# Kernel tuning notes

Hardware: AMD Instinct MI355X
Metric: run time of the kernel (lower is better)

The kernel has to match this reference:

```python
import jax, jax.numpy as jnp
import numpy as np

N, T, P, H, K = 10000, 64, 64, 128, 32
K1, K2 = K // 2, K - K // 2
C = P // 2  # GAT out_channels
E = 320000
EPS = 1e-5


def gru_layer(x, Wih, Whh, bih, bhh):
    # x: [N, T, in]; PyTorch GRU cell semantics
    Hd = Whh.shape[1]
    def step(h, xt):
        gi = xt @ Wih.T + bih            # [N, 3H]
        gh = h @ Whh.T + bhh
        i_r, i_z, i_n = jnp.split(gi, 3, axis=-1)
        h_r, h_z, h_n = jnp.split(gh, 3, axis=-1)
        r = jax.nn.sigmoid(i_r + h_r)
        z = jax.nn.sigmoid(i_z + h_z)
        n = jnp.tanh(i_n + r * h_n)
        h_new = (1.0 - z) * n + z * h
        return h_new, h_new
    h0 = jnp.zeros((x.shape[0], Hd), x.dtype)
    _, ys = jax.lax.scan(step, h0, jnp.swapaxes(x, 0, 1))
    return jnp.swapaxes(ys, 0, 1)


def gru2_last(x, p0, p1):
    y0 = gru_layer(x, *p0)
    y1 = gru_layer(y0, *p1)
    return y1[:, -1, :]


def gat_conv(x, edge_index, W, att_src, att_dst, bias):
    # PyG GATConv, heads=1, concat=False, add_self_loops=True, slope=0.2
    n = x.shape[0]
    h = x @ W                                   # [N, C]
    loops = jnp.arange(n)
    src = jnp.concatenate([edge_index[0], loops])
    dst = jnp.concatenate([edge_index[1], loops])
    a_s = h @ att_src                            # [N]
    a_d = h @ att_dst
    e = jax.nn.leaky_relu(a_s[src] + a_d[dst], 0.2)
    emax = jax.lax.stop_gradient(jax.ops.segment_max(e, dst, num_segments=n))
    ex = jnp.exp(e - emax[dst])
    denom = jax.ops.segment_sum(ex, dst, num_segments=n)
    alpha = ex / denom[dst]
    out = jax.ops.segment_sum(alpha[:, None] * h[src], dst, num_segments=n)
    return out + bias


def batchnorm(x, g, b):
    m = jnp.mean(x, axis=0)
    v = jnp.var(x, axis=0)
    return (x - m) * jax.lax.rsqrt(v + EPS) * g + b


def setup_inputs() -> dict:
    key = jax.random.key(0)
    ks = jax.random.split(key, 40)
    s = 0.05
    d = {}
    d["X_seq"] = jax.random.normal(ks[0], (N, T, P), jnp.float32)
    d["edge_index"] = jax.random.randint(ks[1], (2, E), 0, N, jnp.int64)
    i = 2
    for name, ind in (("gru_t", P), ("gru_cs", P)):
        for l, fin in ((0, ind), (1, H)):
            d[f"{name}_Wih{l}"] = jax.random.normal(ks[i], (3 * H, fin)) * s; i += 1
            d[f"{name}_Whh{l}"] = jax.random.normal(ks[i], (3 * H, H)) * s; i += 1
            d[f"{name}_bih{l}"] = jax.random.normal(ks[i], (3 * H,)) * s; i += 1
            d[f"{name}_bhh{l}"] = jax.random.normal(ks[i], (3 * H,)) * s; i += 1
    d["gat_W"] = jax.random.normal(ks[i], (P, C)) * s; i += 1
    d["gat_att_src"] = jax.random.normal(ks[i], (C,)) * s; i += 1
    d["gat_att_dst"] = jax.random.normal(ks[i], (C,)) * s; i += 1
    d["gat_bias"] = jax.random.normal(ks[i], (C,)) * s; i += 1
    d["proj_t_W"] = jax.random.normal(ks[i], (K1, H)) * s; i += 1
    d["proj_t_b"] = jax.random.normal(ks[i], (K1,)) * s; i += 1
    d["proj_cs_W"] = jax.random.normal(ks[i], (K2, H)) * s; i += 1
    d["proj_cs_b"] = jax.random.normal(ks[i], (K2,)) * s; i += 1
    d["bn1_g"] = jnp.ones((K1,)); d["bn1_b"] = jnp.zeros((K1,))
    d["bn2_g"] = jnp.ones((K2,)); d["bn2_b"] = jnp.zeros((K2,))
    return d


def reference(X_seq, edge_index,
              gru_t_Wih0, gru_t_Whh0, gru_t_bih0, gru_t_bhh0,
              gru_t_Wih1, gru_t_Whh1, gru_t_bih1, gru_t_bhh1,
              gru_cs_Wih0, gru_cs_Whh0, gru_cs_bih0, gru_cs_bhh0,
              gru_cs_Wih1, gru_cs_Whh1, gru_cs_bih1, gru_cs_bhh1,
              gat_W, gat_att_src, gat_att_dst, gat_bias,
              proj_t_W, proj_t_b, proj_cs_W, proj_cs_b,
              bn1_g, bn1_b, bn2_g, bn2_b):
    h_t = gru2_last(X_seq,
                    (gru_t_Wih0, gru_t_Whh0, gru_t_bih0, gru_t_bhh0),
                    (gru_t_Wih1, gru_t_Whh1, gru_t_bih1, gru_t_bhh1))
    X_t = X_seq[:, -1, :]                            # [N, P]
    gat_out = gat_conv(X_t, edge_index, gat_W, gat_att_src, gat_att_dst, gat_bias)
    pad = jnp.zeros((X_t.shape[0], P - C), X_t.dtype)
    residual = X_t - jnp.concatenate([gat_out, pad], axis=1)
    h_cs = gru2_last(residual[:, None, :],
                     (gru_cs_Wih0, gru_cs_Whh0, gru_cs_bih0, gru_cs_bhh0),
                     (gru_cs_Wih1, gru_cs_Whh1, gru_cs_bih1, gru_cs_bhh1))
    f1 = batchnorm(h_t @ proj_t_W.T + proj_t_b, bn1_g, bn1_b)
    f2 = batchnorm(h_cs @ proj_cs_W.T + proj_cs_b, bn2_g, bn2_b)
    return jnp.concatenate([f1, f2], axis=1)
```

## Files before the change

### kernel.cpp

```cpp
#include <hip/hip_runtime.h>
#include <hip/hip_fp16.h>

#define NN 10000
#define TT 64
#define PP 64
#define HH 128
#define EE 320000

typedef _Float16 half8 __attribute__((ext_vector_type(8)));
typedef float f32x4 __attribute__((ext_vector_type(4)));

__device__ __forceinline__ float sigm(float x) {
    return __builtin_amdgcn_rcpf(1.0f + __expf(-x));
}
__device__ __forceinline__ float tanh_(float x) {
    return 1.0f - 2.0f * __builtin_amdgcn_rcpf(__expf(2.0f * x) + 1.0f);
}
__device__ __forceinline__ int hswz(int row, int colbyte) {
    return row * 256 + (colbyte ^ ((row & 7) << 4));
}

__global__ void pack_w_kernel(const float* __restrict__ Wa, int Ka,
                              const float* __restrict__ Wb,
                              _Float16* __restrict__ out, int total) {
    int idx = blockIdx.x * 256 + threadIdx.x;
    if (idx >= total) return;
    int K = Ka + HH;
    int r = idx / K, k = idx - r * K;
    float v = (k < Ka) ? Wa[r * Ka + k] : Wb[r * HH + (k - Ka)];
    out[idx] = (_Float16)v;
}

__global__ __launch_bounds__(512, 2) void gru2_t8_kernel(
    const float* __restrict__ x, int T, int xstride,
    const _Float16* __restrict__ W0,
    const float* __restrict__ bih0, const float* __restrict__ bhh0,
    const _Float16* __restrict__ W1,
    const float* __restrict__ bih1, const float* __restrict__ bhh1,
    float* __restrict__ hout)
{
    __shared__ __align__(16) char lds[65536];
    char* const WX = lds + 16384;
    const int tid = threadIdx.x;
    const int wv = tid >> 6;
    const int lane = tid & 63;
    const int l15 = lane & 15, lg = lane >> 4;
    const int rowbase = blockIdx.x * 16;
    const int col = wv * 16 + l15;

    for (int i = tid; i < 4096; i += 512) ((int*)lds)[i] = 0;

    #pragma unroll
    for (int g = 0; g < 3; ++g) {
        const _Float16* r0 = W0 + ((size_t)((g * 8 + wv) * 16 + l15)) * 192;
        #pragma unroll
        for (int kt = 0; kt < 2; ++kt)
            *(half8*)(WX + wv * 6144 + (g * 2 + kt) * 1024 + lane * 16) =
                *(const half8*)(r0 + kt * 32 + lg * 8);
    }

    half8 w0h[3][4], w1[3][8];
    #pragma unroll
    for (int g = 0; g < 3; ++g) {
        const _Float16* r0 = W0 + ((size_t)((g * 8 + wv) * 16 + l15)) * 192;
        #pragma unroll
        for (int kt = 0; kt < 4; ++kt) w0h[g][kt] = *(const half8*)(r0 + 64 + kt * 32 + lg * 8);
        const _Float16* r1 = W1 + ((size_t)((g * 8 + wv) * 16 + l15)) * 256;
        #pragma unroll
        for (int kt = 0; kt < 8; ++kt) w1[g][kt] = *(const half8*)(r1 + kt * 32 + lg * 8);
    }
    #pragma unroll
    for (int g = 0; g < 3; ++g) {
        #pragma unroll
        for (int kt = 0; kt < 4; ++kt) asm volatile("" : "+a"(w0h[g][kt]));
        #pragma unroll
        for (int kt = 0; kt < 8; ++kt) asm volatile("" : "+a"(w1[g][kt]));
    }

    const float br0  = bih0[col] + bhh0[col];
    const float bz0  = bih0[128 + col] + bhh0[128 + col];
    const float bni0 = bih0[256 + col];
    const float bnh0 = bhh0[256 + col];
    const float br1  = bih1[col] + bhh1[col];
    const float bz1  = bih1[128 + col] + bhh1[128 + col];
    const float bni1 = bih1[256 + col];
    const float bnh1 = bhh1[256 + col];

    const float* xr = x + (size_t)(rowbase + l15) * xstride;

    float hp0[4] = {0.f, 0.f, 0.f, 0.f};
    float hp1[4] = {0.f, 0.f, 0.f, 0.f};

    __syncthreads();

    for (int it = 0; it <= T; ++it) {
        const int off = (it & 1) * 4096;
        char* const H0r = lds + off;
        char* const H0w = lds + (4096 - off);
        char* const H1r = lds + 8192 + off;
        char* const H1w = lds + 8192 + (4096 - off);

        float4 xu0, xv0, xu1, xv1;
        if (it < T) {
            const float* p = xr + it * PP;
            xu0 = *(const float4*)(p + lg * 8);
            xv0 = *(const float4*)(p + lg * 8 + 4);
            xu1 = *(const float4*)(p + 32 + lg * 8);
            xv1 = *(const float4*)(p + 32 + lg * 8 + 4);
        }

        if (it >= 1) {
            f32x4 ar  = {br1, br1, br1, br1};
            f32x4 az  = {bz1, bz1, bz1, bz1};
            f32x4 ani = {bni1, bni1, bni1, bni1};
            f32x4 anh = {bnh1, bnh1, bnh1, bnh1};
            #pragma unroll
            for (int kt = 0; kt < 4; ++kt) {
                const int boff = (kt * 32 + lg * 8) * 2;
                half8 ay  = *(const half8*)(H0r + hswz(l15, boff));
                half8 ah1 = *(const half8*)(H1r + hswz(l15, boff));
                ar  = __builtin_amdgcn_mfma_f32_16x16x32_f16(ay,  w1[0][kt],   ar, 0,0,0);
                ar  = __builtin_amdgcn_mfma_f32_16x16x32_f16(ah1, w1[0][4+kt], ar, 0,0,0);
                az  = __builtin_amdgcn_mfma_f32_16x16x32_f16(ay,  w1[1][kt],   az, 0,0,0);
                az  = __builtin_amdgcn_mfma_f32_16x16x32_f16(ah1, w1[1][4+kt], az, 0,0,0);
                ani = __builtin_amdgcn_mfma_f32_16x16x32_f16(ay,  w1[2][kt],   ani, 0,0,0);
                anh = __builtin_amdgcn_mfma_f32_16x16x32_f16(ah1, w1[2][4+kt], anh, 0,0,0);
            }
            #pragma unroll
            for (int r = 0; r < 4; ++r) {
                float rg = sigm(ar[r]);
                float zg = sigm(az[r]);
                float ng = tanh_(ani[r] + rg * anh[r]);
                float hv = ng + zg * (hp1[r] - ng);
                hp1[r] = hv;
                *(_Float16*)(H1w + hswz(lg * 4 + r, col * 2)) = (_Float16)hv;
            }
        }

        if (it < T) {
            half8 ax0, ax1;
            ax0[0]=(_Float16)xu0.x; ax0[1]=(_Float16)xu0.y; ax0[2]=(_Float16)xu0.z; ax0[3]=(_Float16)xu0.w;
            ax0[4]=(_Float16)xv0.x; ax0[5]=(_Float16)xv0.y; ax0[6]=(_Float16)xv0.z; ax0[7]=(_Float16)xv0.w;
            ax1[0]=(_Float16)xu1.x; ax1[1]=(_Float16)xu1.y; ax1[2]=(_Float16)xu1.z; ax1[3]=(_Float16)xu1.w;
            ax1[4]=(_Float16)xv1.x; ax1[5]=(_Float16)xv1.y; ax1[6]=(_Float16)xv1.z; ax1[7]=(_Float16)xv1.w;
            f32x4 ar  = {br0, br0, br0, br0};
            f32x4 az  = {bz0, bz0, bz0, bz0};
            f32x4 ani = {bni0, bni0, bni0, bni0};
            f32x4 anh = {bnh0, bnh0, bnh0, bnh0};
            #pragma unroll
            for (int kt = 0; kt < 2; ++kt) {
                const char* wb = WX + wv * 6144 + kt * 1024 + lane * 16;
                half8 wxr = *(const half8*)(wb);
                half8 wxz = *(const half8*)(wb + 2048);
                half8 wxn = *(const half8*)(wb + 4096);
                half8 ax = (kt == 0) ? ax0 : ax1;
                ar  = __builtin_amdgcn_mfma_f32_16x16x32_f16(ax, wxr, ar, 0,0,0);
                az  = __builtin_amdgcn_mfma_f32_16x16x32_f16(ax, wxz, az, 0,0,0);
                ani = __builtin_amdgcn_mfma_f32_16x16x32_f16(ax, wxn, ani, 0,0,0);
            }
            #pragma unroll
            for (int kt = 0; kt < 4; ++kt) {
                half8 ah = *(const half8*)(H0r + hswz(l15, (kt * 32 + lg * 8) * 2));
                ar  = __builtin_amdgcn_mfma_f32_16x16x32_f16(ah, w0h[0][kt], ar, 0,0,0);
                az  = __builtin_amdgcn_mfma_f32_16x16x32_f16(ah, w0h[1][kt], az, 0,0,0);
                anh = __builtin_amdgcn_mfma_f32_16x16x32_f16(ah, w0h[2][kt], anh, 0,0,0);
            }
            #pragma unroll
            for (int r = 0; r < 4; ++r) {
                float rg = sigm(ar[r]);
                float zg = sigm(az[r]);
                float ng = tanh_(ani[r] + rg * anh[r]);
                float hv = ng + zg * (hp0[r] - ng);
                hp0[r] = hv;
                *(_Float16*)(H0w + hswz(lg * 4 + r, col * 2)) = (_Float16)hv;
            }
        }
        __syncthreads();
    }

    #pragma unroll
    for (int r = 0; r < 4; ++r)
        hout[(size_t)(rowbase + lg * 4 + r) * HH + col] = hp1[r];
}

__global__ void gat_node_kernel(const float* __restrict__ Xseq, const float* __restrict__ W,
                                const float* __restrict__ att_s, const float* __restrict__ att_d,
                                float* __restrict__ h, float* __restrict__ a_s, float* __restrict__ a_d,
                                float* __restrict__ denom, float* __restrict__ accum) {
    __shared__ float sW[64][33];
    __shared__ float sas[32], sad[32];
    int tid = threadIdx.x;
    for (int i = tid; i < 64 * 32; i += 256) sW[i >> 5][i & 31] = W[i];
    if (tid < 32) { sas[tid] = att_s[tid]; sad[tid] = att_d[tid]; }
    __syncthreads();
    int c = tid & 31;
    int n = blockIdx.x * 8 + (tid >> 5);
    const float* xr = Xseq + (size_t)n * (TT * PP) + 63 * PP;
    float acc = 0.f;
    #pragma unroll
    for (int k = 0; k < 64; ++k) acc += xr[k] * sW[k][c];
    h[n * 32 + c] = acc;
    accum[n * 32 + c] = 0.f;
    float ps = acc * sas[c];
    float pd = acc * sad[c];
    #pragma unroll
    for (int m = 16; m > 0; m >>= 1) { ps += __shfl_xor(ps, m, 32); pd += __shfl_xor(pd, m, 32); }
    if (c == 0) { a_s[n] = ps; a_d[n] = pd; denom[n] = 0.f; }
}

__global__ void gat_edge_kernel(const int* __restrict__ ei,
                                const float* __restrict__ a_s, const float* __restrict__ a_d,
                                const float* __restrict__ h,
                                float* __restrict__ denom, float* __restrict__ accum) {
    int gid = blockIdx.x * 256 + threadIdx.x;
    int e = gid >> 5, c = gid & 31;
    if (e >= EE + NN) return;
    int src, dst;
    if (e < EE) { src = ei[e]; dst = ei[EE + e]; }
    else        { src = e - EE; dst = src; }
    float s = a_s[src] + a_d[dst];
    float le = (s > 0.f) ? s : 0.2f * s;
    float ex = __expf(le);
    unsafeAtomicAdd(&accum[dst * 32 + c], ex * h[src * 32 + c]);
    if (c == 0) unsafeAtomicAdd(&denom[dst], ex);
}

__global__ void residual_kernel(const float* __restrict__ Xseq, const float* __restrict__ accum,
                                const float* __restrict__ denom, const float* __restrict__ bias,
                                float* __restrict__ res) {
    int idx = blockIdx.x * 256 + threadIdx.x;
    if (idx >= NN * 64) return;
    int n = idx >> 6, k = idx & 63;
    float xv = Xseq[(size_t)n * (TT * PP) + 63 * PP + k];
    float g = 0.f;
    if (k < 32) g = accum[n * 32 + k] / denom[n] + bias[k];
    res[idx] = xv - g;
}

__global__ void proj_kernel(const float* __restrict__ ht, const float* __restrict__ hcs,
                            const float* __restrict__ Wt, const float* __restrict__ bt,
                            const float* __restrict__ Wc, const float* __restrict__ bc,
                            float* __restrict__ out) {
    __shared__ float sW[32][129];
    __shared__ float sb[32];
    int tid = threadIdx.x;
    for (int i = tid; i < 16 * 128; i += 256) {
        sW[i >> 7][i & 127] = Wt[i];
        sW[16 + (i >> 7)][i & 127] = Wc[i];
    }
    if (tid < 16) { sb[tid] = bt[tid]; sb[16 + tid] = bc[tid]; }
    __syncthreads();
    int idx = blockIdx.x * 256 + tid;
    int n = idx >> 5, c = idx & 31;
    const float* hrow = ((c < 16) ? ht : hcs) + (size_t)n * HH;
    const float* wrow = sW[c];
    float acc = sb[c];
    #pragma unroll 8
    for (int k = 0; k < 128; ++k) acc += hrow[k] * wrow[k];
    out[idx] = acc;
}

__global__ void bn_stats_kernel(const float* __restrict__ raw,
                                const float* __restrict__ g1, const float* __restrict__ b1,
                                const float* __restrict__ g2, const float* __restrict__ b2,
                                float* __restrict__ ss) {
    int c = blockIdx.x;
    int tid = threadIdx.x;
    float s = 0.f, q = 0.f;
    for (int n = tid; n < NN; n += 256) {
        float v = raw[n * 32 + c];
        s += v; q += v * v;
    }
    __shared__ float ls[256], lq[256];
    ls[tid] = s; lq[tid] = q;
    __syncthreads();
    for (int st = 128; st > 0; st >>= 1) {
        if (tid < st) { ls[tid] += ls[tid + st]; lq[tid] += lq[tid + st]; }
        __syncthreads();
    }
    if (tid == 0) {
        float m = ls[0] / (float)NN;
        float var = lq[0] / (float)NN - m * m;
        float istd = rsqrtf(var + 1e-5f);
        float gg = (c < 16) ? g1[c] : g2[c - 16];
        float bb = (c < 16) ? b1[c] : b2[c - 16];
        float sc = istd * gg;
        ss[c] = sc;
        ss[32 + c] = bb - m * sc;
    }
}

__global__ void bn_apply_kernel(float* __restrict__ out, const float* __restrict__ ss) {
    int idx = blockIdx.x * 256 + threadIdx.x;
    if (idx >= NN * 32) return;
    int c = idx & 31;
    out[idx] = out[idx] * ss[c] + ss[32 + c];
}

extern "C" void kernel_launch(void* const* d_in, const int* in_sizes, int n_in,
                              void* d_out, int out_size, void* d_ws, size_t ws_size,
                              hipStream_t stream) {
    const float* Xseq  = (const float*)d_in[0];
    const int*   ei    = (const int*)d_in[1];
    const float* tWih0 = (const float*)d_in[2];
    const float* tWhh0 = (const float*)d_in[3];
    const float* tbih0 = (const float*)d_in[4];
    const float* tbhh0 = (const float*)d_in[5];
    const float* tWih1 = (const float*)d_in[6];
    const float* tWhh1 = (const float*)d_in[7];
    const float* tbih1 = (const float*)d_in[8];
    const float* tbhh1 = (const float*)d_in[9];
    const float* cWih0 = (const float*)d_in[10];
    const float* cWhh0 = (const float*)d_in[11];
    const float* cbih0 = (const float*)d_in[12];
    const float* cbhh0 = (const float*)d_in[13];
    const float* cWih1 = (const float*)d_in[14];
    const float* cWhh1 = (const float*)d_in[15];
    const float* cbih1 = (const float*)d_in[16];
    const float* cbhh1 = (const float*)d_in[17];
    const float* gatW  = (const float*)d_in[18];
    const float* atts  = (const float*)d_in[19];
    const float* attd  = (const float*)d_in[20];
    const float* gatb  = (const float*)d_in[21];
    const float* ptW   = (const float*)d_in[22];
    const float* ptb   = (const float*)d_in[23];
    const float* pcW   = (const float*)d_in[24];
    const float* pcb   = (const float*)d_in[25];
    const float* bn1g  = (const float*)d_in[26];
    const float* bn1b  = (const float*)d_in[27];
    const float* bn2g  = (const float*)d_in[28];
    const float* bn2b  = (const float*)d_in[29];

    char* ws = (char*)d_ws;
    _Float16* Wt0 = (_Float16*)(ws);
    _Float16* Wt1 = (_Float16*)(ws + 147456);
    _Float16* Wc0 = (_Float16*)(ws + 344064);
    _Float16* Wc1 = (_Float16*)(ws + 491520);
    float* h_t   = (float*)(ws + 688128);
    float* h_cs  = (float*)(ws + 5808128);
    float* gath  = (float*)(ws + 10928128);
    float* a_s   = (float*)(ws + 12208128);
    float* a_d   = (float*)(ws + 12248128);
    float* denom = (float*)(ws + 12288128);
    float* accum = (float*)(ws + 12328128);
    float* resid = (float*)(ws + 13608128);
    float* ss    = (float*)(ws + 16168128);

    pack_w_kernel<<<288, 256, 0, stream>>>(tWih0, 64,  tWhh0, Wt0, 384 * 192);
    pack_w_kernel<<<384, 256, 0, stream>>>(tWih1, 128, tWhh1, Wt1, 384 * 256);
    pack_w_kernel<<<288, 256, 0, stream>>>(cWih0, 64,  cWhh0, Wc0, 384 * 192);
    pack_w_kernel<<<384, 256, 0, stream>>>(cWih1, 128, cWhh1, Wc1, 384 * 256);

    gru2_t8_kernel<<<625, 512, 0, stream>>>(Xseq, TT, TT * PP, Wt0, tbih0, tbhh0,
                                            Wt1, tbih1, tbhh1, h_t);

    gat_node_kernel<<<1250, 256, 0, stream>>>(Xseq, gatW, atts, attd, gath, a_s, a_d, denom, accum);
    gat_edge_kernel<<<41250, 256, 0, stream>>>(ei, a_s, a_d, gath, denom, accum);
    residual_kernel<<<2500, 256, 0, stream>>>(Xseq, accum, denom, gatb, resid);

    gru2_t8_kernel<<<625, 512, 0, stream>>>(resid, 1, PP, Wc0, cbih0, cbhh0,
                                            Wc1, cbih1, cbhh1, h_cs);

    proj_kernel<<<1250, 256, 0, stream>>>(h_t, h_cs, ptW, ptb, pcW, pcb, (float*)d_out);
    bn_stats_kernel<<<32, 256, 0, stream>>>((const float*)d_out, bn1g, bn1b, bn2g, bn2b, ss);
    bn_apply_kernel<<<1250, 256, 0, stream>>>((float*)d_out, ss);
}
```

Before: 528.4 us.

## Process 48 rows per GRU block to amortize register-resident weights

Each GRU block now handles three 16-row M-fragments (48 rows) instead of one, reusing the register- and LDS-resident weights across more rows per sync step. The launch drops from 625 to 209 blocks and uses 96KB of dynamic LDS, with launch bounds lowered to one block per SIMD set. The previous hidden state is now read back from LDS in fp16 instead of kept in fp32 registers, which frees registers but adds rounding of the recurrent state. With 209 blocks on a 256-CU part, some CUs sit idle and occupancy is lower, so latency hiding depends on the three independent fragments.

After: 765.0 us. 1.45x slower.

```diff
diff --git a/kernel.cpp b/kernel.cpp
--- a/kernel.cpp
+++ b/kernel.cpp
@@ -31,7 +31,7 @@
     out[idx] = (_Float16)v;
 }
 
-__global__ __launch_bounds__(512, 2) void gru2_t8_kernel(
+__global__ __launch_bounds__(512, 1) void gru2_t8_kernel(
     const float* __restrict__ x, int T, int xstride,
     const _Float16* __restrict__ W0,
     const float* __restrict__ bih0, const float* __restrict__ bhh0,
@@ -39,16 +39,18 @@
     const float* __restrict__ bih1, const float* __restrict__ bhh1,
     float* __restrict__ hout)
 {
-    __shared__ __align__(16) char lds[65536];
-    char* const WX = lds + 16384;
+    extern __shared__ __align__(16) char lds[];
+    char* const H0B = lds;
+    char* const H1B = lds + 24576;
+    char* const WX  = lds + 49152;
     const int tid = threadIdx.x;
     const int wv = tid >> 6;
     const int lane = tid & 63;
     const int l15 = lane & 15, lg = lane >> 4;
-    const int rowbase = blockIdx.x * 16;
+    const int rowbase = blockIdx.x * 48;
     const int col = wv * 16 + l15;
 
-    for (int i = tid; i < 4096; i += 512) ((int*)lds)[i] = 0;
+    for (int i = tid; i < 12288; i += 512) ((int*)lds)[i] = 0;
 
     #pragma unroll
     for (int g = 0; g < 3; ++g) {
@@ -86,101 +88,111 @@
     const float bni1 = bih1[256 + col];
     const float bnh1 = bhh1[256 + col];
 
-    const float* xr = x + (size_t)(rowbase + l15) * xstride;
-
-    float hp0[4] = {0.f, 0.f, 0.f, 0.f};
-    float hp1[4] = {0.f, 0.f, 0.f, 0.f};
+    const float* xr[3];
+    #pragma unroll
+    for (int mf = 0; mf < 3; ++mf) {
+        int rr = rowbase + mf * 16 + l15;
+        if (rr > NN - 1) rr = NN - 1;
+        xr[mf] = x + (size_t)rr * xstride;
+    }
 
     __syncthreads();
 
     for (int it = 0; it <= T; ++it) {
-        const int off = (it & 1) * 4096;
-        char* const H0r = lds + off;
-        char* const H0w = lds + (4096 - off);
-        char* const H1r = lds + 8192 + off;
-        char* const H1w = lds + 8192 + (4096 - off);
-
-        float4 xu0, xv0, xu1, xv1;
-        if (it < T) {
-            const float* p = xr + it * PP;
-            xu0 = *(const float4*)(p + lg * 8);
-            xv0 = *(const float4*)(p + lg * 8 + 4);
-            xu1 = *(const float4*)(p + 32 + lg * 8);
-            xv1 = *(const float4*)(p + 32 + lg * 8 + 4);
-        }
-
-        if (it >= 1) {
-            f32x4 ar  = {br1, br1, br1, br1};
-            f32x4 az  = {bz1, bz1, bz1, bz1};
-            f32x4 ani = {bni1, bni1, bni1, bni1};
-            f32x4 anh = {bnh1, bnh1, bnh1, bnh1};
-            #pragma unroll
-            for (int kt = 0; kt < 4; ++kt) {
-                const int boff = (kt * 32 + lg * 8) * 2;
-                half8 ay  = *(const half8*)(H0r + hswz(l15, boff));
-                half8 ah1 = *(const half8*)(H1r + hswz(l15, boff));
-                ar  = __builtin_amdgcn_mfma_f32_16x16x32_f16(ay,  w1[0][kt],   ar, 0,0,0);
-                ar  = __builtin_amdgcn_mfma_f32_16x16x32_f16(ah1, w1[0][4+kt], ar, 0,0,0);
-                az  = __builtin_amdgcn_mfma_f32_16x16x32_f16(ay,  w1[1][kt],   az, 0,0,0);
-                az  = __builtin_amdgcn_mfma_f32_16x16x32_f16(ah1, w1[1][4+kt], az, 0,0,0);
-                ani = __builtin_amdgcn_mfma_f32_16x16x32_f16(ay,  w1[2][kt],   ani, 0,0,0);
-                anh = __builtin_amdgcn_mfma_f32_16x16x32_f16(ah1, w1[2][4+kt], anh, 0,0,0);
+        const int off = (it & 1) * 12288;
+        char* const H0r = H0B + off;
+        char* const H0w = H0B + (12288 - off);
+        char* const H1r = H1B + off;
+        char* const H1w = H1B + (12288 - off);
+
+        #pragma unroll
+        for (int mf = 0; mf < 3; ++mf) {
+            const int arow = mf * 16 + l15;
+
+            float4 xu0, xv0, xu1, xv1;
+            if (it < T) {
+                const float* p = xr[mf] + it * PP;
+                xu0 = *(const float4*)(p + lg * 8);
+                xv0 = *(const float4*)(p + lg * 8 + 4);
+                xu1 = *(const float4*)(p + 32 + lg * 8);
+                xv1 = *(const float4*)(p + 32 + lg * 8 + 4);
             }
-            #pragma unroll
-            for (int r = 0; r < 4; ++r) {
-                float rg = sigm(ar[r]);
-                float zg = sigm(az[r]);
-                float ng = tanh_(ani[r] + rg * anh[r]);
-                float hv = ng + zg * (hp1[r] - ng);
-                hp1[r] = hv;
-                *(_Float16*)(H1w + hswz(lg * 4 + r, col * 2)) = (_Float16)hv;
+
+            if (it >= 1) {
+                f32x4 ar  = {br1, br1, br1, br1};
+                f32x4 az  = {bz1, bz1, bz1, bz1};
+                f32x4 ani = {bni1, bni1, bni1, bni1};
+                f32x4 anh = {bnh1, bnh1, bnh1, bnh1};
+                #pragma unroll
+                for (int kt = 0; kt < 4; ++kt) {
+                    const int boff = (kt * 32 + lg * 8) * 2;
+                    half8 ay  = *(const half8*)(H0r + hswz(arow, boff));
+                    half8 ah1 = *(const half8*)(H1r + hswz(arow, boff));
+                    ar  = __builtin_amdgcn_mfma_f32_16x16x32_f16(ay,  w1[0][kt],   ar, 0,0,0);
+                    ar  = __builtin_amdgcn_mfma_f32_16x16x32_f16(ah1, w1[0][4+kt], ar, 0,0,0);
+                    az  = __builtin_amdgcn_mfma_f32_16x16x32_f16(ay,  w1[1][kt],   az, 0,0,0);
+                    az  = __builtin_amdgcn_mfma_f32_16x16x32_f16(ah1, w1[1][4+kt], az, 0,0,0);
+                    ani = __builtin_amdgcn_mfma_f32_16x16x32_f16(ay,  w1[2][kt],   ani, 0,0,0);
+                    anh = __builtin_amdgcn_mfma_f32_16x16x32_f16(ah1, w1[2][4+kt], anh, 0,0,0);
+                }
+                #pragma unroll
+                for (int r = 0; r < 4; ++r) {
+                    const int drow = mf * 16 + lg * 4 + r;
+                    float hold = (float)(*(const _Float16*)(H1r + hswz(drow, col * 2)));
+                    float rg = sigm(ar[r]);
+                    float zg = sigm(az[r]);
+                    float ng = tanh_(ani[r] + rg * anh[r]);
+                    float hv = ng + zg * (hold - ng);
+                    *(_Float16*)(H1w + hswz(drow, col * 2)) = (_Float16)hv;
+                    if (it == T) {
+                        const int grow = rowbase + drow;
+                        if (grow < NN) hout[(size_t)grow * HH + col] = hv;
+                    }
+                }
             }
-        }
-
-        if (it < T) {
-            half8 ax0, ax1;
-            ax0[0]=(_Float16)xu0.x; ax0[1]=(_Float16)xu0.y; ax0[2]=(_Float16)xu0.z; ax0[3]=(_Float16)xu0.w;
-            ax0[4]=(_Float16)xv0.x; ax0[5]=(_Float16)xv0.y; ax0[6]=(_Float16)xv0.z; ax0[7]=(_Float16)xv0.w;
-            ax1[0]=(_Float16)xu1.x; ax1[1]=(_Float16)xu1.y; ax1[2]=(_Float16)xu1.z; ax1[3]=(_Float16)xu1.w;
-            ax1[4]=(_Float16)xv1.x; ax1[5]=(_Float16)xv1.y; ax1[6]=(_Float16)xv1.z; ax1[7]=(_Float16)xv1.w;
-            f32x4 ar  = {br0, br0, br0, br0};
-            f32x4 az  = {bz0, bz0, bz0, bz0};
-            f32x4 ani = {bni0, bni0, bni0, bni0};
-            f32x4 anh = {bnh0, bnh0, bnh0, bnh0};
-            #pragma unroll
-            for (int kt = 0; kt < 2; ++kt) {
-                const char* wb = WX + wv * 6144 + kt * 1024 + lane * 16;
-                half8 wxr = *(const half8*)(wb);
-                half8 wxz = *(const half8*)(wb + 2048);
-                half8 wxn = *(const half8*)(wb + 4096);
-                half8 ax = (kt == 0) ? ax0 : ax1;
-                ar  = __builtin_amdgcn_mfma_f32_16x16x32_f16(ax, wxr, ar, 0,0,0);
-                az  = __builtin_amdgcn_mfma_f32_16x16x32_f16(ax, wxz, az, 0,0,0);
-                ani = __builtin_amdgcn_mfma_f32_16x16x32_f16(ax, wxn, ani, 0,0,0);
-            }
-            #pragma unroll
-            for (int kt = 0; kt < 4; ++kt) {
-                half8 ah = *(const half8*)(H0r + hswz(l15, (kt * 32 + lg * 8) * 2));
-                ar  = __builtin_amdgcn_mfma_f32_16x16x32_f16(ah, w0h[0][kt], ar, 0,0,0);
-                az  = __builtin_amdgcn_mfma_f32_16x16x32_f16(ah, w0h[1][kt], az, 0,0,0);
-                anh = __builtin_amdgcn_mfma_f32_16x16x32_f16(ah, w0h[2][kt], anh, 0,0,0);
-            }
-            #pragma unroll
-            for (int r = 0; r < 4; ++r) {
-                float rg = sigm(ar[r]);
-                float zg = sigm(az[r]);
-                float ng = tanh_(ani[r] + rg * anh[r]);
-                float hv = ng + zg * (hp0[r] - ng);
-                hp0[r] = hv;
-                *(_Float16*)(H0w + hswz(lg * 4 + r, col * 2)) = (_Float16)hv;
+
+            if (it < T) {
+                half8 ax0, ax1;
+                ax0[0]=(_Float16)xu0.x; ax0[1]=(_Float16)xu0.y; ax0[2]=(_Float16)xu0.z; ax0[3]=(_Float16)xu0.w;
+                ax0[4]=(_Float16)xv0.x; ax0[5]=(_Float16)xv0.y; ax0[6]=(_Float16)xv0.z; ax0[7]=(_Float16)xv0.w;
+                ax1[0]=(_Float16)xu1.x; ax1[1]=(_Float16)xu1.y; ax1[2]=(_Float16)xu1.z; ax1[3]=(_Float16)xu1.w;
+                ax1[4]=(_Float16)xv1.x; ax1[5]=(_Float16)xv1.y; ax1[6]=(_Float16)xv1.z; ax1[7]=(_Float16)xv1.w;
+                f32x4 ar  = {br0, br0, br0, br0};
+                f32x4 az  = {bz0, bz0, bz0, bz0};
+                f32x4 ani = {bni0, bni0, bni0, bni0};
+                f32x4 anh = {bnh0, bnh0, bnh0, bnh0};
+                #pragma unroll
+                for (int kt = 0; kt < 2; ++kt) {
+                    const char* wb = WX + wv * 6144 + kt * 1024 + lane * 16;
+                    half8 wxr = *(const half8*)(wb);
+                    half8 wxz = *(const half8*)(wb + 2048);
+                    half8 wxn = *(const half8*)(wb + 4096);
+                    half8 ax = (kt == 0) ? ax0 : ax1;
+                    ar  = __builtin_amdgcn_mfma_f32_16x16x32_f16(ax, wxr, ar, 0,0,0);
+                    az  = __builtin_amdgcn_mfma_f32_16x16x32_f16(ax, wxz, az, 0,0,0);
+                    ani = __builtin_amdgcn_mfma_f32_16x16x32_f16(ax, wxn, ani, 0,0,0);
+                }
+                #pragma unroll
+                for (int kt = 0; kt < 4; ++kt) {
+                    half8 ah = *(const half8*)(H0r + hswz(arow, (kt * 32 + lg * 8) * 2));
+                    ar  = __builtin_amdgcn_mfma_f32_16x16x32_f16(ah, w0h[0][kt], ar, 0,0,0);
+                    az  = __builtin_amdgcn_mfma_f32_16x16x32_f16(ah, w0h[1][kt], az, 0,0,0);
+                    anh = __builtin_amdgcn_mfma_f32_16x16x32_f16(ah, w0h[2][kt], anh, 0,0,0);
+                }
+                #pragma unroll
+                for (int r = 0; r < 4; ++r) {
+                    const int drow = mf * 16 + lg * 4 + r;
+                    float hold = (float)(*(const _Float16*)(H0r + hswz(drow, col * 2)));
+                    float rg = sigm(ar[r]);
+                    float zg = sigm(az[r]);
+                    float ng = tanh_(ani[r] + rg * anh[r]);
+                    float hv = ng + zg * (hold - ng);
+                    *(_Float16*)(H0w + hswz(drow, col * 2)) = (_Float16)hv;
+                }
             }
         }
         __syncthreads();
     }
-
-    #pragma unroll
-    for (int r = 0; r < 4; ++r)
-        hout[(size_t)(rowbase + lg * 4 + r) * HH + col] = hp1[r];
 }
 
 __global__ void gat_node_kernel(const float* __restrict__ Xseq, const float* __restrict__ W,
@@ -346,20 +358,23 @@
     float* resid = (float*)(ws + 13608128);
     float* ss    = (float*)(ws + 16168128);
 
+    (void)hipFuncSetAttribute((const void*)gru2_t8_kernel,
+                              hipFuncAttributeMaxDynamicSharedMemorySize, 98304);
+
     pack_w_kernel<<<288, 256, 0, stream>>>(tWih0, 64,  tWhh0, Wt0, 384 * 192);
     pack_w_kernel<<<384, 256, 0, stream>>>(tWih1, 128, tWhh1, Wt1, 384 * 256);
     pack_w_kernel<<<288, 256, 0, stream>>>(cWih0, 64,  cWhh0, Wc0, 384 * 192);
     pack_w_kernel<<<384, 256, 0, stream>>>(cWih1, 128, cWhh1, Wc1, 384 * 256);
 
-    gru2_t8_kernel<<<625, 512, 0, stream>>>(Xseq, TT, TT * PP, Wt0, tbih0, tbhh0,
-                                            Wt1, tbih1, tbhh1, h_t);
+    gru2_t8_kernel<<<209, 512, 98304, stream>>>(Xseq, TT, TT * PP, Wt0, tbih0, tbhh0,
+                                                Wt1, tbih1, tbhh1, h_t);
 
     gat_node_kernel<<<1250, 256, 0, stream>>>(Xseq, gatW, atts, attd, gath, a_s, a_d, denom, accum);
     gat_edge_kernel<<<41250, 256, 0, stream>>>(ei, a_s, a_d, gath, denom, accum);
     residual_kernel<<<2500, 256, 0, stream>>>(Xseq, accum, denom, gatb, resid);
 
-    gru2_t8_kernel<<<625, 512, 0, stream>>>(resid, 1, PP, Wc0, cbih0, cbhh0,
-                                            Wc1, cbih1, cbhh1, h_cs);
+    gru2_t8_kernel<<<209, 512, 98304, stream>>>(resid, 1, PP, Wc0, cbih0, cbhh0,
+                                                Wc1, cbih1, cbhh1, h_cs);
 
     proj_kernel<<<1250, 256, 0, stream>>>(h_t, h_cs, ptW, ptb, pcW, pcb, (float*)d_out);
     bn_stats_kernel<<<32, 256, 0, stream>>>((const float*)d_out, bn1g, bn1b, bn2g, bn2b, ss);
```
